# Performance work log

Hardware: AMD Instinct MI355X
Metric: run time of the kernel (lower is better)

## Reference

```python
import jax, jax.numpy as jnp
import numpy as np

N = 2_000_000   # total flattened logits (anchors x classes scale)
FG = 256        # number of foreground (targets==1) entries
DELTA = 1.0


def setup_inputs() -> dict:
    key = jax.random.key(0)
    k1, k2 = jax.random.split(key)
    logits = jax.random.normal(k1, (N,), dtype=jnp.float32)
    fg_idx = jax.random.choice(k2, N, shape=(FG,), replace=False)
    targets = jnp.zeros((N,), dtype=jnp.int32).at[fg_idx].set(1)
    return {"logits": logits, "targets": targets, "fg_num": FG}


def _ap_loss(logits, targets, fg_num):
    """Faithful port of AP_loss: returns (loss [1], grad [N]).

    The torch validity filter (targets==0 & logits >= min(fg)-delta) is
    redundant: for invalid bg, (l - fg_i)/(2*delta)+0.5 < 0, so clamp gives 0.
    We therefore mask with (targets==0) over the full array (static shapes).
    """
    bg_mask = (targets == 0).astype(logits.dtype)
    fg_idx = jnp.nonzero(targets == 1, size=fg_num)[0]
    fg_logits = logits[fg_idx]            # [fg]
    order = jnp.argsort(fg_logits)
    sorted_fg = fg_logits[order]          # ascending, matches torch loop order

    inv2d = 1.0 / (2.0 * DELTA)

    def step(carry, f_i):
        max_prec, bg_grad = carry
        tmp1 = jnp.clip((fg_logits - f_i) * inv2d + 0.5, 0.0, 1.0)   # [fg]
        tmp2 = jnp.clip((logits - f_i) * inv2d + 0.5, 0.0, 1.0) * bg_mask  # [N]
        a = jnp.sum(tmp1) + 0.5
        b = jnp.sum(tmp2)
        cur = a / (a + b)
        new_max = jnp.maximum(max_prec, cur)
        scale = jnp.where(max_prec <= cur, 1.0, (1.0 - max_prec) / (1.0 - cur))
        bg_grad = bg_grad + tmp2 * (scale / (a + b))
        return (new_max, bg_grad), new_max

    init = (jnp.zeros((), logits.dtype), jnp.zeros_like(logits))
    (_, bg_grad), prec_sorted = jax.lax.scan(step, init, sorted_fg)

    prec = jnp.zeros((fg_num,), logits.dtype).at[order].set(prec_sorted)
    grad = bg_grad.at[fg_idx].set(-(1.0 - prec))
    denom = max(fg_num, 1)
    grad = grad / denom
    metric = jnp.sum(prec, keepdims=True) / denom   # [1]
    return 1.0 - metric, grad


def reference(logits, targets, fg_num):
    loss, _ = _ap_loss(logits, targets, fg_num)
    return loss
```

## Files before the change

kernel.cpp:

```cpp
#include <hip/hip_runtime.h>

#define FG    256
#define NBIN  1024
#define BINV  32.0f
#define BOFF  512.0f
#define QSCL  1048576.0f
#define SUMQ  33554432.0f

typedef unsigned long long u64;


__global__ void init_kernel(int* counter, u64* gacc) {
    int tid = threadIdx.x;
    if (tid == 0) *counter = 0;
    gacc[tid] = 0ull;
}

__global__ void __launch_bounds__(1024) hist_kernel(
        const float* __restrict__ logits,
        const int* __restrict__ targets,
        int* __restrict__ counter,
        float* __restrict__ fgraw,
        u64* __restrict__ gacc, int n) {
    __shared__ u64 h[NBIN];
    const int tid = threadIdx.x;
    h[tid] = 0ull;
    __syncthreads();

    const int n4 = n >> 2;
    const float4* l4 = (const float4*)logits;
    const int4*   t4 = (const int4*)targets;
    const int stride = gridDim.x * blockDim.x;
    for (int i = blockIdx.x * blockDim.x + tid; i < n4; i += stride) {
        float4 x = l4[i];
        int4   t = t4[i];
        #pragma unroll
        for (int e = 0; e < 4; ++e) {
            float l  = (e == 0) ? x.x : (e == 1) ? x.y : (e == 2) ? x.z : x.w;
            int   tg = (e == 0) ? t.x : (e == 1) ? t.y : (e == 2) ? t.z : t.w;
            float u = fmaf(l, BINV, BOFF);
            u = fminf(fmaxf(u, 0.f), 1023.0f);
            int   b    = (int)u;
            float frac = u - (float)b;
            unsigned int qoff = (unsigned int)(frac * QSCL + 0.5f);
            u64 pk = (1ull << 42) | (u64)qoff;
            atomicAdd(&h[b], pk);
            if (tg == 1) {
                int p = atomicAdd(counter, 1);
                fgraw[p] = l;
            }
        }
    }
    if (blockIdx.x == 0 && tid == 0) {
        for (int i = n4 << 2; i < n; ++i) {
            float l = logits[i];
            float u = fmaf(l, BINV, BOFF);
            u = fminf(fmaxf(u, 0.f), 1023.0f);
            int   b    = (int)u;
            float frac = u - (float)b;
            unsigned int qoff = (unsigned int)(frac * QSCL + 0.5f);
            atomicAdd(&h[b], (1ull << 42) | (u64)qoff);
            if (targets[i] == 1) { int p = atomicAdd(counter, 1); fgraw[p] = l; }
        }
    }
    __syncthreads();
    u64 v = h[tid];
    if (v) atomicAdd(&gacc[tid], v);
}

__global__ void __launch_bounds__(1024) final_kernel(
        const float* __restrict__ fgraw,
        const u64* __restrict__ gacc,
        float* __restrict__ out, int n) {
    __shared__ float rc[NBIN], rs[NBIN];
    __shared__ float pc[NBIN], ps[NBIN];
    __shared__ float sfv[FG], sf[FG];
    __shared__ float wc[16], ws[16];
    __shared__ float wm[4], wsum[4];
    const int tid  = threadIdx.x;
    const int lane = tid & 63;
    const int wv   = tid >> 6;

    {
        u64 v = gacc[tid];
        float cnt = (float)(v >> 42);
        float qs  = (float)(v & ((1ull << 42) - 1ull));
        float binlo = ((float)tid - BOFF) * (1.0f / BINV);
        rc[tid] = cnt;
        rs[tid] = fmaf(qs, 1.0f / SUMQ, binlo * cnt);
    }
    if (tid < FG) sfv[tid] = fgraw[tid];
    __syncthreads();

    float c = rc[tid], s = rs[tid];
    #pragma unroll
    for (int off = 1; off < 64; off <<= 1) {
        float tc = __shfl_up(c, off, 64), ts = __shfl_up(s, off, 64);
        if (lane >= off) { c += tc; s += ts; }
    }
    if (lane == 63) { wc[wv] = c; ws[wv] = s; }
    __syncthreads();
    if (wv == 0 && lane < 16) {
        float cc = wc[lane], ss = ws[lane];
        #pragma unroll
        for (int off = 1; off < 16; off <<= 1) {
            float tc = __shfl_up(cc, off, 64), ts = __shfl_up(ss, off, 64);
            if (lane >= off) { cc += tc; ss += ts; }
        }
        wc[lane] = cc; ws[lane] = ss;
    }
    __syncthreads();
    if (wv > 0) { c += wc[wv - 1]; s += ws[wv - 1]; }
    pc[tid] = c; ps[tid] = s;

    if (tid < FG) {
        float v = sfv[tid];
        int r = 0;
        for (int j = 0; j < FG; ++j) {
            float o = sfv[j];
            r += (o < v || (o == v && j < tid)) ? 1 : 0;
        }
        sf[r] = v;
    }
    __syncthreads();

    float cur = 0.f;
    if (tid < FG) {
        const float fi = sf[tid];
        float a = 0.5f;
        for (int j = 0; j < FG; ++j) {
            float v = (sf[j] - fi) * 0.5f + 0.5f;
            a += fminf(fmaxf(v, 0.f), 1.f);
        }
        float C[2], S[2];
        #pragma unroll
        for (int q = 0; q < 2; ++q) {
            float t = (q == 0) ? (fi - 1.0f) : (fi + 1.0f);
            float u = fmaf(t, BINV, BOFF);
            u = fminf(fmaxf(u, 0.f), 1023.0f);
            float kf = floorf(u);
            int   k  = (int)kf;
            float frac = u - kf;
            C[q] = pc[k] + rc[k] * (frac - 1.0f);
            S[q] = ps[k] + rs[k] * (frac - 1.0f);
        }
        const float Cab   = (float)n - C[1];
        const float Cw    = C[1] - C[0];
        const float Sw    = S[1] - S[0];
        const float b_all = Cab + 0.5f * Sw + (0.5f - 0.5f * fi) * Cw;
        const float b_bg  = b_all - (a - 0.5f);
        cur = a / (a + b_bg);
    }
    if (tid < FG) {
        float m = cur;
        #pragma unroll
        for (int off = 1; off < 64; off <<= 1) {
            float t = __shfl_up(m, off, 64);
            if (lane >= off) m = fmaxf(m, t);
        }
        if (lane == 63) wm[wv] = m;
        __syncthreads();
        float pmax = -1.f;
        for (int w = 0; w < 4; ++w) if (w < wv) pmax = fmaxf(pmax, wm[w]);
        m = fmaxf(m, pmax);
        float v = m;
        #pragma unroll
        for (int off = 32; off; off >>= 1) v += __shfl_down(v, off, 64);
        if (lane == 0) wsum[wv] = v;
    } else {
        __syncthreads();
    }
    __syncthreads();
    if (tid == 0) {
        float t = (wsum[0] + wsum[1]) + (wsum[2] + wsum[3]);
        out[0] = 1.f - t / (float)FG;
    }
}

extern "C" void kernel_launch(void* const* d_in, const int* in_sizes, int n_in,
                              void* d_out, int out_size, void* d_ws, size_t ws_size,
                              hipStream_t stream) {
    const float* logits  = (const float*)d_in[0];
    const int*   targets = (const int*)d_in[1];
    const int n = in_sizes[0];

    char*  wb      = (char*)d_ws;
    int*   counter = (int*)wb;
    float* fgraw   = (float*)(wb + 256);
    u64*   gacc    = (u64*)(wb + 2048);
    float* out     = (float*)d_out;

    init_kernel<<<1, NBIN, 0, stream>>>(counter, gacc);
    hist_kernel<<<256, 1024, 0, stream>>>(logits, targets, counter, fgraw, gacc, n);
    final_kernel<<<1, NBIN, 0, stream>>>(fgraw, gacc, out, n);
}
```

Measured before the change: 86.78 us.

## Use 32-bit shared histogram atomics and split FG rank/sum loops across all threads

The shared-memory histogram switches from 64-bit packed atomics to 32-bit packed atomics. The count sits in the high bits and a 5-bit quantized in-bin offset in the low bits, and each bin is widened to 64 bits only for the single global atomic per bin. This targets the cost of 64-bit LDS atomics in the hot loop over 2M elements, at the price of much coarser offset precision, which adds error to the interpolated sums. The final kernel also spreads the 256x256 rank and pairwise-clamp loops across all 1024 threads in four chunks, reducing the serial work done by only 256 threads. It tidies the barriers so __syncthreads is no longer called inside a divergent branch.

```diff
diff --git a/kernel.cpp b/kernel.cpp
--- a/kernel.cpp
+++ b/kernel.cpp
@@ -4,10 +4,9 @@
 #define NBIN  1024
 #define BINV  32.0f
 #define BOFF  512.0f
-#define QSCL  1048576.0f
-#define SUMQ  33554432.0f
 
 typedef unsigned long long u64;
+typedef unsigned int u32;
 
 
 __global__ void init_kernel(int* counter, u64* gacc) {
@@ -22,9 +21,9 @@
         int* __restrict__ counter,
         float* __restrict__ fgraw,
         u64* __restrict__ gacc, int n) {
-    __shared__ u64 h[NBIN];
+    __shared__ u32 h[NBIN];
     const int tid = threadIdx.x;
-    h[tid] = 0ull;
+    h[tid] = 0u;
     __syncthreads();
 
     const int n4 = n >> 2;
@@ -39,12 +38,10 @@
             float l  = (e == 0) ? x.x : (e == 1) ? x.y : (e == 2) ? x.z : x.w;
             int   tg = (e == 0) ? t.x : (e == 1) ? t.y : (e == 2) ? t.z : t.w;
             float u = fmaf(l, BINV, BOFF);
-            u = fminf(fmaxf(u, 0.f), 1023.0f);
-            int   b    = (int)u;
-            float frac = u - (float)b;
-            unsigned int qoff = (unsigned int)(frac * QSCL + 0.5f);
-            u64 pk = (1ull << 42) | (u64)qoff;
-            atomicAdd(&h[b], pk);
+            u = fminf(fmaxf(u, 0.f), 1023.99f);
+            int b = (int)u;
+            u32 qoff = (u32)((u - (float)b) * 32.0f);
+            atomicAdd(&h[b], (1u << 18) | qoff);
             if (tg == 1) {
                 int p = atomicAdd(counter, 1);
                 fgraw[p] = l;
@@ -55,17 +52,19 @@
         for (int i = n4 << 2; i < n; ++i) {
             float l = logits[i];
             float u = fmaf(l, BINV, BOFF);
-            u = fminf(fmaxf(u, 0.f), 1023.0f);
-            int   b    = (int)u;
-            float frac = u - (float)b;
-            unsigned int qoff = (unsigned int)(frac * QSCL + 0.5f);
-            atomicAdd(&h[b], (1ull << 42) | (u64)qoff);
+            u = fminf(fmaxf(u, 0.f), 1023.99f);
+            int b = (int)u;
+            u32 qoff = (u32)((u - (float)b) * 32.0f);
+            atomicAdd(&h[b], (1u << 18) | qoff);
             if (targets[i] == 1) { int p = atomicAdd(counter, 1); fgraw[p] = l; }
         }
     }
     __syncthreads();
-    u64 v = h[tid];
-    if (v) atomicAdd(&gacc[tid], v);
+    u32 v = h[tid];
+    if (v) {
+        u64 pk = ((u64)(v >> 18) << 32) | (u64)(v & 0x3FFFFu);
+        atomicAdd(&gacc[tid], pk);
+    }
 }
 
 __global__ void __launch_bounds__(1024) final_kernel(
@@ -75,6 +74,8 @@
     __shared__ float rc[NBIN], rs[NBIN];
     __shared__ float pc[NBIN], ps[NBIN];
     __shared__ float sfv[FG], sf[FG];
+    __shared__ int   pr[1024];
+    __shared__ float pa[1024];
     __shared__ float wc[16], ws[16];
     __shared__ float wm[4], wsum[4];
     const int tid  = threadIdx.x;
@@ -83,11 +84,11 @@
 
     {
         u64 v = gacc[tid];
-        float cnt = (float)(v >> 42);
-        float qs  = (float)(v & ((1ull << 42) - 1ull));
+        float cnt = (float)(u32)(v >> 32);
+        float qs  = (float)(u32)(v & 0xFFFFFFFFull);
         float binlo = ((float)tid - BOFF) * (1.0f / BINV);
         rc[tid] = cnt;
-        rs[tid] = fmaf(qs, 1.0f / SUMQ, binlo * cnt);
+        rs[tid] = fmaf(qs + 0.5f * cnt, 1.0f / 1024.0f, binlo * cnt);
     }
     if (tid < FG) sfv[tid] = fgraw[tid];
     __syncthreads();
@@ -99,7 +100,20 @@
         if (lane >= off) { c += tc; s += ts; }
     }
     if (lane == 63) { wc[wv] = c; ws[wv] = s; }
-    __syncthreads();
+
+    {
+        int i = tid & 255, ch = tid >> 8;
+        float v = sfv[i];
+        int r = 0;
+        #pragma unroll 8
+        for (int j = ch * 64; j < ch * 64 + 64; ++j) {
+            float o = sfv[j];
+            r += (o < v || (o == v && j < i)) ? 1 : 0;
+        }
+        pr[tid] = r;
+    }
+    __syncthreads();
+
     if (wv == 0 && lane < 16) {
         float cc = wc[lane], ss = ws[lane];
         #pragma unroll
@@ -109,35 +123,37 @@
         }
         wc[lane] = cc; ws[lane] = ss;
     }
+    if (tid < FG) {
+        int r = pr[tid] + pr[tid + 256] + pr[tid + 512] + pr[tid + 768];
+        sf[r] = sfv[tid];
+    }
     __syncthreads();
     if (wv > 0) { c += wc[wv - 1]; s += ws[wv - 1]; }
     pc[tid] = c; ps[tid] = s;
 
-    if (tid < FG) {
-        float v = sfv[tid];
-        int r = 0;
-        for (int j = 0; j < FG; ++j) {
-            float o = sfv[j];
-            r += (o < v || (o == v && j < tid)) ? 1 : 0;
-        }
-        sf[r] = v;
+    {
+        int i = tid & 255, ch = tid >> 8;
+        float fi = sf[i];
+        float sum = 0.f;
+        #pragma unroll 8
+        for (int j = ch * 64; j < ch * 64 + 64; ++j) {
+            float v = (sf[j] - fi) * 0.5f + 0.5f;
+            sum += fminf(fmaxf(v, 0.f), 1.f);
+        }
+        pa[tid] = sum;
     }
     __syncthreads();
 
     float cur = 0.f;
     if (tid < FG) {
         const float fi = sf[tid];
-        float a = 0.5f;
-        for (int j = 0; j < FG; ++j) {
-            float v = (sf[j] - fi) * 0.5f + 0.5f;
-            a += fminf(fmaxf(v, 0.f), 1.f);
-        }
+        const float a = 0.5f + pa[tid] + pa[tid + 256] + pa[tid + 512] + pa[tid + 768];
         float C[2], S[2];
         #pragma unroll
         for (int q = 0; q < 2; ++q) {
             float t = (q == 0) ? (fi - 1.0f) : (fi + 1.0f);
             float u = fmaf(t, BINV, BOFF);
-            u = fminf(fmaxf(u, 0.f), 1023.0f);
+            u = fminf(fmaxf(u, 0.f), 1023.99f);
             float kf = floorf(u);
             int   k  = (int)kf;
             float frac = u - kf;
@@ -150,8 +166,6 @@
         const float b_all = Cab + 0.5f * Sw + (0.5f - 0.5f * fi) * Cw;
         const float b_bg  = b_all - (a - 0.5f);
         cur = a / (a + b_bg);
-    }
-    if (tid < FG) {
         float m = cur;
         #pragma unroll
         for (int off = 1; off < 64; off <<= 1) {
@@ -159,7 +173,11 @@
             if (lane >= off) m = fmaxf(m, t);
         }
         if (lane == 63) wm[wv] = m;
-        __syncthreads();
+        pr[tid] = __float_as_int(m);
+    }
+    __syncthreads();
+    if (tid < FG) {
+        float m = __int_as_float(pr[tid]);
         float pmax = -1.f;
         for (int w = 0; w < 4; ++w) if (w < wv) pmax = fmaxf(pmax, wm[w]);
         m = fmaxf(m, pmax);
@@ -167,8 +185,6 @@
         #pragma unroll
         for (int off = 32; off; off >>= 1) v += __shfl_down(v, off, 64);
         if (lane == 0) wsum[wv] = v;
-    } else {
-        __syncthreads();
     }
     __syncthreads();
     if (tid == 0) {
```

New measurement: 80.14 us (median of 2 runs). -7.6%, faster.
